# Performance work log

Measured on AMD Instinct MI355X. Metric: run time of the kernel, lower is better.

## Reference

```python
import jax, jax.numpy as jnp
import numpy as np

B, L, D, K = 8, 1024, 1024, 128
VOCAB, N_ATOM_FEAT, N_TIMESTEPS = 160, 512, 1000
NEG = jnp.finfo(jnp.float32).min
SCALING = K ** (-0.5)


def setup_inputs() -> dict:
    key = jax.random.key(0)
    ks = jax.random.split(key, 14)
    inp = {}
    # forward args
    inp["token_id"] = jax.random.randint(ks[0], (B, L), 0, VOCAB)  # 0 => padding
    inp["node_attr"] = jax.random.randint(ks[1], (B, L, 9), 0, N_ATOM_FEAT)
    inp["is_molecule"] = jax.random.randint(ks[2], (B,), 0, 2).astype(bool)
    inp["pos"] = jax.random.normal(ks[3], (B, L, 3), jnp.float32) * 10.0
    inp["time_step"] = jax.random.randint(ks[4], (B, L), 0, N_TIMESTEPS)
    # learned parameters
    inp["embed_table"] = jax.random.normal(ks[5], (VOCAB, D), jnp.float32) * 0.02
    inp["atom_feat_table"] = jax.random.normal(ks[6], (N_ATOM_FEAT, D), jnp.float32) * 0.02
    inp["time_table"] = jax.random.normal(ks[7], (N_TIMESTEPS, D), jnp.float32) * 0.02
    inp["time_w1"] = jax.random.normal(ks[8], (D, D), jnp.float32) * (D ** -0.5)
    inp["time_b1"] = jnp.zeros((D,), jnp.float32)
    inp["time_w2"] = jax.random.normal(ks[9], (D, D), jnp.float32) * (D ** -0.5)
    inp["time_b2"] = jnp.zeros((D,), jnp.float32)
    inp["pos_emb_w"] = jax.random.normal(ks[10], (1, K), jnp.float32)          # Linear(1 -> K), no bias
    inp["pos_feature_w"] = jax.random.normal(ks[11], (K, D), jnp.float32) * (K ** -0.5)  # Linear(K -> D), no bias
    return inp


def _pos_emb(pos, padding_mask, pos_emb_w, pos_feature_w):
    # pos: [B,L,3], padding_mask: [B,L] bool
    delta = pos[:, :, None, :] - pos[:, None, :, :]          # [B,L,L,3]
    dist = 1.0 / (jnp.linalg.norm(delta, axis=-1) + 1.0)     # [B,L,L]
    # masked_fill on key side (expand_mask) and query side (padding_mask)
    mask = padding_mask[:, None, :] | padding_mask[:, :, None]
    dist = jnp.where(mask, NEG, dist)
    # value projection: Linear(1->K) on per-atom radial norm, zeroed at padding
    pe = jnp.linalg.norm(pos, axis=-1, keepdims=True) @ pos_emb_w  # [B,L,K]
    pe = jnp.where(padding_mask[:, :, None], 0.0, pe)
    attn = jax.nn.softmax(dist * SCALING, axis=-1)            # [B,L,L]
    pfe = jnp.einsum("bqk,bkc->bqc", attn, pe)                 # [B,L,K]
    pfe = pfe @ pos_feature_w                                  # [B,L,D]
    return jnp.where(padding_mask[:, :, None], 0.0, pfe)


def reference(token_id, node_attr, is_molecule, pos, time_step,
              embed_table, atom_feat_table, time_table,
              time_w1, time_b1, time_w2, time_b2,
              pos_emb_w, pos_feature_w):
    padding_mask = token_id == 0                               # [B,L]
    x = embed_table[token_id]                                  # [B,L,D]
    # 2D atom features: embed cols 1: and sum over feature axis
    atom_emb = atom_feat_table[node_attr[:, :, 1:]].sum(axis=-2)  # [B,L,D]
    atom_emb = jnp.where(is_molecule[:, None, None], atom_emb, 0.0)
    x = x + atom_emb
    # time step encoder: learnable embedding + Linear-SiLU-Linear MLP
    t = time_table[time_step]                                   # [B,L,D]
    time_embed = jax.nn.silu(t @ time_w1 + time_b1) @ time_w2 + time_b2
    x = x + time_embed
    # pairwise 3D positional embedding (softmax attention over 1/(r+1))
    x = x + _pos_emb(pos, padding_mask, pos_emb_w, pos_feature_w)
    return x, padding_mask
```

## Files before the change

### kernel.cpp

```cpp
#include <hip/hip_runtime.h>
#include <hip/hip_bf16.h>
#include <math.h>

#define BB 8
#define LL 1024
#define DD 1024
#define KK 128
#define NTS 1000
#define SCALE 0.08838834764831845f

typedef __attribute__((ext_vector_type(8))) short short8;
typedef __attribute__((ext_vector_type(4))) float f32x4;

__device__ __forceinline__ unsigned short f2bf(float x) {
    __hip_bfloat16 h = __float2bfloat16(x);
    return *reinterpret_cast<unsigned short*>(&h);
}
__device__ __forceinline__ float bf2f(unsigned short u) {
    return __uint_as_float(((unsigned int)u) << 16);
}

__device__ __forceinline__ void gload_lds16(const void* g, void* l) {
    __builtin_amdgcn_global_load_lds(
        (const __attribute__((address_space(1))) unsigned int*)g,
        (__attribute__((address_space(3))) unsigned int*)l, 16, 0, 0);
}

union SMem {
    float4 keys[LL];
    float  tile[32][33];
};

__device__ __forceinline__ void transpose_tile(
    const float* __restrict__ in, unsigned short* __restrict__ out,
    int idx, SMem& sm)
{
    const int tid = threadIdx.x;
    const int bx = (idx & 31) * 32, by = (idx >> 5) * 32;
    const int tx = tid & 31, ty = tid >> 5;
    #pragma unroll
    for (int r = 0; r < 32; r += 8)
        sm.tile[ty + r][tx] = in[(size_t)(by + ty + r) * DD + bx + tx];
    __syncthreads();
    #pragma unroll
    for (int r = 0; r < 32; r += 8)
        out[(size_t)(bx + ty + r) * DD + by + tx] = f2bf(sm.tile[tx][ty + r]);
    __syncthreads();
}

template<bool AF32>
__device__ __forceinline__ void gemm64(
    const float* __restrict__ Af, const unsigned short* __restrict__ Ab,
    const unsigned short* __restrict__ Bt, const float* __restrict__ bias,
    unsigned short* __restrict__ Cout, int mBase, int nBase, bool do_silu)
{
    __shared__ __align__(16) unsigned short As[2][64 * 64];
    __shared__ __align__(16) unsigned short Bs[2][64 * 64];

    const int tid  = threadIdx.x;
    const int lane = tid & 63, wave = tid >> 6;
    const int wm = wave >> 1, wn = wave & 1;
    const int quad = lane >> 4, l16 = lane & 15;
    const int c0 = wave * 2;

    int rowA[2], kEl[2], rAc[2];
    #pragma unroll
    for (int i = 0; i < 2; ++i) {
        const int c   = c0 + i;
        const int o   = c * 1024 + lane * 16;
        const int row = o >> 7;
        const int lin = o ^ ((row & 7) << 4);
        rowA[i] = row;
        kEl[i]  = (lin & 127) >> 1;
        if (AF32) {
            int r = mBase + row;
            rAc[i] = r < NTS ? r : NTS - 1;
        }
    }

    f32x4 acc[2][2];
    #pragma unroll
    for (int i = 0; i < 2; ++i)
        #pragma unroll
        for (int j = 0; j < 2; ++j)
            acc[i][j] = (f32x4){0.f, 0.f, 0.f, 0.f};

    float4 pa[2][2];

    if (AF32) {
        #pragma unroll
        for (int i = 0; i < 2; ++i) {
            const float* p = Af + (size_t)rAc[i] * DD + kEl[i];
            pa[i][0] = *(const float4*)p;
            pa[i][1] = *(const float4*)(p + 4);
        }
    } else {
        #pragma unroll
        for (int i = 0; i < 2; ++i)
            gload_lds16(Ab + (size_t)(mBase + rowA[i]) * DD + kEl[i],
                        (char*)&As[0][0] + (c0 + i) * 1024);
    }
    #pragma unroll
    for (int i = 0; i < 2; ++i)
        gload_lds16(Bt + (size_t)(nBase + rowA[i]) * DD + kEl[i],
                    (char*)&Bs[0][0] + (c0 + i) * 1024);
    asm volatile("s_waitcnt vmcnt(0)" ::: "memory");
    if (AF32) {
        #pragma unroll
        for (int i = 0; i < 2; ++i) {
            short8 s;
            s[0] = f2bf(pa[i][0].x); s[1] = f2bf(pa[i][0].y);
            s[2] = f2bf(pa[i][0].z); s[3] = f2bf(pa[i][0].w);
            s[4] = f2bf(pa[i][1].x); s[5] = f2bf(pa[i][1].y);
            s[6] = f2bf(pa[i][1].z); s[7] = f2bf(pa[i][1].w);
            *(short8*)((char*)&As[0][0] + (c0 + i) * 1024 + lane * 16) = s;
        }
    }
    __syncthreads();

    int buf = 0;
    for (int t = 0; t < 16; ++t) {
        const int kn = (t + 1) * 64;
        if (t < 15) {
            if (AF32) {
                #pragma unroll
                for (int i = 0; i < 2; ++i) {
                    const float* p = Af + (size_t)rAc[i] * DD + kn + kEl[i];
                    pa[i][0] = *(const float4*)p;
                    pa[i][1] = *(const float4*)(p + 4);
                }
            } else {
                #pragma unroll
                for (int i = 0; i < 2; ++i)
                    gload_lds16(Ab + (size_t)(mBase + rowA[i]) * DD + kn + kEl[i],
                                (char*)&As[buf ^ 1][0] + (c0 + i) * 1024);
            }
            #pragma unroll
            for (int i = 0; i < 2; ++i)
                gload_lds16(Bt + (size_t)(nBase + rowA[i]) * DD + kn + kEl[i],
                            (char*)&Bs[buf ^ 1][0] + (c0 + i) * 1024);
        }

        #pragma unroll
        for (int kk = 0; kk < 64; kk += 32) {
            short8 a[2], b[2];
            #pragma unroll
            for (int i = 0; i < 2; ++i) {
                const int row  = wm * 32 + i * 16 + l16;
                const int byte = ((row << 7) + ((kk + quad * 8) << 1))
                                 ^ ((row & 7) << 4);
                a[i] = *(const short8*)((const char*)&As[buf][0] + byte);
            }
            #pragma unroll
            for (int j = 0; j < 2; ++j) {
                const int row  = wn * 32 + j * 16 + l16;
                const int byte = ((row << 7) + ((kk + quad * 8) << 1))
                                 ^ ((row & 7) << 4);
                b[j] = *(const short8*)((const char*)&Bs[buf][0] + byte);
            }
            #pragma unroll
            for (int i = 0; i < 2; ++i)
                #pragma unroll
                for (int j = 0; j < 2; ++j)
                    acc[i][j] = __builtin_amdgcn_mfma_f32_16x16x32_bf16(
                                    a[i], b[j], acc[i][j], 0, 0, 0);
        }

        if (t < 15) {
            asm volatile("s_waitcnt vmcnt(0)" ::: "memory");
            if (AF32) {
                #pragma unroll
                for (int i = 0; i < 2; ++i) {
                    short8 s;
                    s[0] = f2bf(pa[i][0].x); s[1] = f2bf(pa[i][0].y);
                    s[2] = f2bf(pa[i][0].z); s[3] = f2bf(pa[i][0].w);
                    s[4] = f2bf(pa[i][1].x); s[5] = f2bf(pa[i][1].y);
                    s[6] = f2bf(pa[i][1].z); s[7] = f2bf(pa[i][1].w);
                    *(short8*)((char*)&As[buf ^ 1][0] + (c0 + i) * 1024 + lane * 16) = s;
                }
            }
            __syncthreads();
        }
        buf ^= 1;
    }

    #pragma unroll
    for (int j = 0; j < 2; ++j) {
        const int col = nBase + wn * 32 + j * 16 + l16;
        const float bv = bias[col];
        #pragma unroll
        for (int i = 0; i < 2; ++i) {
            #pragma unroll
            for (int r = 0; r < 4; ++r) {
                const int row = mBase + wm * 32 + i * 16 + quad * 4 + r;
                float val = acc[i][j][r] + bv;
                if (do_silu) val = val / (1.0f + __expf(-val));
                Cout[(size_t)row * DD + col] = f2bf(val);
            }
        }
    }
}

__global__ __launch_bounds__(256) void prep(
    const float* __restrict__ w1,
    const float* __restrict__ w2,
    const float* __restrict__ embed_f,
    const float* __restrict__ atom_f,
    const float* __restrict__ pos_emb_w,
    const float* __restrict__ pos_feature_w,
    const void*  __restrict__ is_mol_raw,
    const int*   __restrict__ token_id,
    const float* __restrict__ pos,
    unsigned short* __restrict__ W1t,
    unsigned short* __restrict__ W2t,
    unsigned short* __restrict__ embed_bf,
    unsigned short* __restrict__ atom_bf,
    float* __restrict__ v,
    int*   __restrict__ is_mol_out,
    float* __restrict__ sSg)
{
    __shared__ SMem sm;
    const int blk = blockIdx.x;
    const int tid = threadIdx.x;

    if (blk < 1024) {
        transpose_tile(w1, W1t, blk, sm);
    } else if (blk < 2048) {
        transpose_tile(w2, W2t, blk - 1024, sm);
    } else if (blk < 2208) {
        const int e = ((blk - 2048) * 256 + tid) * 4;
        float4 vv = *(const float4*)&embed_f[e];
        ushort4 o = { f2bf(vv.x), f2bf(vv.y), f2bf(vv.z), f2bf(vv.w) };
        *(ushort4*)&embed_bf[e] = o;
    } else if (blk < 2720) {
        const int e = ((blk - 2208) * 256 + tid) * 4;
        float4 vv = *(const float4*)&atom_f[e];
        ushort4 o = { f2bf(vv.x), f2bf(vv.y), f2bf(vv.z), f2bf(vv.w) };
        *(ushort4*)&atom_bf[e] = o;
    } else if (blk < 2724) {
        const int d = (blk - 2720) * 256 + tid;
        float acc = 0.0f;
        #pragma unroll 4
        for (int c = 0; c < KK; ++c)
            acc += pos_emb_w[c] * pos_feature_w[c * DD + d];
        v[d] = acc;
    } else if (blk == 2724) {
        if (tid == 0) {
            const int* ip = (const int*)is_mol_raw;
            const unsigned char* cp = (const unsigned char*)is_mol_raw;
            bool all_bin = true;
            for (int i = 0; i < BB; ++i) {
                int x = ip[i];
                if (x != 0 && x != 1) all_bin = false;
            }
            for (int i = 0; i < BB; ++i)
                is_mol_out[i] = all_bin ? (ip[i] != 0) : (cp[i] != 0);
        }
    } else {
        const int ab = blk - 2725;
        const int batch = ab >> 6;
        const int q0 = (ab & 63) * 16;
        const int lane = tid & 63, wave = tid >> 6;

        #pragma unroll
        for (int i = 0; i < 4; ++i) {
            const int k = tid + i * 256;
            const int t = batch * LL + k;
            const float x = pos[t * 3 + 0];
            const float y = pos[t * 3 + 1];
            const float z = pos[t * 3 + 2];
            const int tok = token_id[t];
            const float n = sqrtf(x * x + y * y + z * z);
            sm.keys[k] = make_float4(x, y, z, tok == 0 ? -1.0f : n);
        }
        __syncthreads();

        #pragma unroll
        for (int qi = 0; qi < 4; ++qi) {
            const int ql = wave * 4 + qi;
            const float4 qk = sm.keys[q0 + ql];
            float lsum = 0.0f, lws = 0.0f;
            #pragma unroll 4
            for (int i = 0; i < 16; ++i) {
                const float4 kd = sm.keys[lane + i * 64];
                const float dx = qk.x - kd.x, dy = qk.y - kd.y, dz = qk.z - kd.z;
                const float dn = sqrtf(dx * dx + dy * dy + dz * dz);
                const float e = __expf(SCALE / (dn + 1.0f));
                const bool valid = kd.w >= 0.0f;
                const float ev = valid ? e : 0.0f;
                lsum += ev;
                lws  += ev * (valid ? kd.w : 0.0f);
            }
            #pragma unroll
            for (int off = 32; off > 0; off >>= 1) {
                lsum += __shfl_xor(lsum, off);
                lws  += __shfl_xor(lws,  off);
            }
            if (lane == 0)
                sSg[batch * LL + q0 + ql] = (qk.w < 0.0f) ? 0.0f : (lws / lsum);
        }
    }
}

__global__ __launch_bounds__(256) void gemm1k(
    const float* __restrict__ time_table,
    const unsigned short* __restrict__ W1t,
    const float* __restrict__ b1,
    unsigned short* __restrict__ H)
{
    const int b = (blockIdx.x & 7) * 32 + (blockIdx.x >> 3);
    gemm64<true>(time_table, nullptr, W1t, b1, H,
                 (b >> 4) * 64, (b & 15) * 64, true);
}

__global__ __launch_bounds__(256) void gemm2k(
    const unsigned short* __restrict__ H,
    const unsigned short* __restrict__ W2t,
    const float* __restrict__ b2,
    unsigned short* __restrict__ Ebf)
{
    const int b = (blockIdx.x & 7) * 32 + (blockIdx.x >> 3);
    gemm64<false>(nullptr, H, W2t, b2, Ebf,
                  (b >> 4) * 64, (b & 15) * 64, false);
}

__global__ __launch_bounds__(256) void assemble(
    const int*   __restrict__ token_id,
    const int*   __restrict__ node_attr,
    const int*   __restrict__ time_step,
    const unsigned short* __restrict__ embed_bf,
    const unsigned short* __restrict__ atom_bf,
    const unsigned short* __restrict__ Ebf,
    const float* __restrict__ v,
    const float* __restrict__ sSg,
    const int*   __restrict__ is_mol,
    float* __restrict__ out)
{
    const int blk   = blockIdx.x;
    const int batch = blk >> 7;
    const int q0    = (blk & 127) << 3;
    const int tid   = threadIdx.x;

    const int im   = is_mol[batch];
    const int half = tid >> 7;
    const int tl   = tid & 127;
    const int j    = tl * 8;
    const float4 v0 = *(const float4*)&v[j];
    const float4 v1 = *(const float4*)&v[j + 4];

    #pragma unroll
    for (int qp = 0; qp < 4; ++qp) {
        const int ql  = qp * 2 + half;
        const int t   = batch * LL + q0 + ql;
        const int tok = token_id[t];
        const int ts  = time_step[t];
        const float s = sSg[t];

        float o[8];
        short8 eb = *(const short8*)&embed_bf[(size_t)tok * DD + j];
        #pragma unroll
        for (int d = 0; d < 8; ++d) o[d] = bf2f((unsigned short)eb[d]);

        if (im) {
            #pragma unroll
            for (int f = 1; f < 9; ++f) {
                const int a = node_attr[t * 9 + f];
                short8 ab = *(const short8*)&atom_bf[(size_t)a * DD + j];
                #pragma unroll
                for (int d = 0; d < 8; ++d) o[d] += bf2f((unsigned short)ab[d]);
            }
        }
        short8 er = *(const short8*)&Ebf[(size_t)ts * DD + j];
        #pragma unroll
        for (int d = 0; d < 8; ++d) o[d] += bf2f((unsigned short)er[d]);

        o[0] += s * v0.x; o[1] += s * v0.y; o[2] += s * v0.z; o[3] += s * v0.w;
        o[4] += s * v1.x; o[5] += s * v1.y; o[6] += s * v1.z; o[7] += s * v1.w;

        float4 wlo = {o[0], o[1], o[2], o[3]};
        float4 whi = {o[4], o[5], o[6], o[7]};
        *(float4*)&out[(size_t)t * DD + j]     = wlo;
        *(float4*)&out[(size_t)t * DD + j + 4] = whi;
    }

    if (tid < 8) {
        const int t = batch * LL + q0 + tid;
        out[(size_t)BB * LL * DD + t] = (token_id[t] == 0) ? 1.0f : 0.0f;
    }
}

extern "C" void kernel_launch(void* const* d_in, const int* in_sizes, int n_in,
                              void* d_out, int out_size, void* d_ws, size_t ws_size,
                              hipStream_t stream)
{
    const int*   token_id      = (const int*)  d_in[0];
    const int*   node_attr     = (const int*)  d_in[1];
    const void*  is_mol_raw    = (const void*) d_in[2];
    const float* pos           = (const float*)d_in[3];
    const int*   time_step     = (const int*)  d_in[4];
    const float* embed_table   = (const float*)d_in[5];
    const float* atom_feat     = (const float*)d_in[6];
    const float* time_table    = (const float*)d_in[7];
    const float* w1            = (const float*)d_in[8];
    const float* b1            = (const float*)d_in[9];
    const float* w2            = (const float*)d_in[10];
    const float* b2            = (const float*)d_in[11];
    const float* pos_emb_w     = (const float*)d_in[12];
    const float* pos_feature_w = (const float*)d_in[13];

    float* out = (float*)d_out;
    char*  ws  = (char*)d_ws;

    unsigned short* W1t      = (unsigned short*)(ws);
    unsigned short* Ebf      = (unsigned short*)(ws);
    unsigned short* H        = (unsigned short*)(ws + (2u << 20));
    unsigned short* W2t      = (unsigned short*)(ws + (4u << 20));
    unsigned short* embed_bf = (unsigned short*)(ws + (6u << 20));
    unsigned short* atom_bf  = (unsigned short*)(ws + (6u << 20) + (512u << 10));
    char*           base7    = ws + (7u << 20) + (512u << 10);
    float*          V        = (float*)(base7);
    float*          sSg      = (float*)(base7 + (4u << 10));
    int*            is_mol_r = (int*)  (base7 + (36u << 10));

    prep<<<3237, 256, 0, stream>>>(w1, w2, embed_table, atom_feat,
                                   pos_emb_w, pos_feature_w,
                                   is_mol_raw, token_id, pos,
                                   W1t, W2t, embed_bf, atom_bf,
                                   V, is_mol_r, sSg);

    gemm1k<<<256, 256, 0, stream>>>(time_table, W1t, b1, H);

    gemm2k<<<256, 256, 0, stream>>>(H, W2t, b2, Ebf);

    assemble<<<1024, 256, 0, stream>>>(token_id, node_attr, time_step,
                                       embed_bf, atom_bf, Ebf, V, sSg,
                                       is_mol_r, out);
}
```

Before: 154.2 us.

## Fuse first time-MLP GEMM into prep kernel reading untransposed fp32 W1

Removes the separate W1 transpose and the gemm1 launch. The first GEMM now runs as 256 blocks inside the prep kernel, loading fp32 W1 directly into LDS and converting to bf16 when forming MFMA B fragments. This cuts one launch and the W1 transpose round trip through memory, and lets GEMM1 overlap with the other prep work. In exchange, the B tile is fp32 in LDS (twice the footprint), the per-element strided LDS reads and conversions in the inner loop may add bank conflicts and ALU work, and the larger shared-memory union can lower occupancy for all prep blocks.

```diff
diff --git a/kernel.cpp b/kernel.cpp
--- a/kernel.cpp
+++ b/kernel.cpp
@@ -26,57 +26,58 @@
         (__attribute__((address_space(3))) unsigned int*)l, 16, 0, 0);
 }
 
-union SMem {
+union SMemD1 {
+    struct {
+        unsigned short As[2][64 * 64];
+        float          Bs[2][64 * 64];
+    } g;
     float4 keys[LL];
     float  tile[32][33];
 };
 
 __device__ __forceinline__ void transpose_tile(
     const float* __restrict__ in, unsigned short* __restrict__ out,
-    int idx, SMem& sm)
+    int idx, float (*tile)[33])
 {
     const int tid = threadIdx.x;
     const int bx = (idx & 31) * 32, by = (idx >> 5) * 32;
     const int tx = tid & 31, ty = tid >> 5;
     #pragma unroll
     for (int r = 0; r < 32; r += 8)
-        sm.tile[ty + r][tx] = in[(size_t)(by + ty + r) * DD + bx + tx];
+        tile[ty + r][tx] = in[(size_t)(by + ty + r) * DD + bx + tx];
     __syncthreads();
     #pragma unroll
     for (int r = 0; r < 32; r += 8)
-        out[(size_t)(bx + ty + r) * DD + by + tx] = f2bf(sm.tile[tx][ty + r]);
+        out[(size_t)(bx + ty + r) * DD + by + tx] = f2bf(tile[tx][ty + r]);
     __syncthreads();
 }
 
-template<bool AF32>
-__device__ __forceinline__ void gemm64(
-    const float* __restrict__ Af, const unsigned short* __restrict__ Ab,
-    const unsigned short* __restrict__ Bt, const float* __restrict__ bias,
-    unsigned short* __restrict__ Cout, int mBase, int nBase, bool do_silu)
+__device__ __forceinline__ void gemm1_tile(
+    const float* __restrict__ Af, const float* __restrict__ W1,
+    const float* __restrict__ bias, unsigned short* __restrict__ Cout,
+    int mBase, int nBase, SMemD1& sm)
 {
-    __shared__ __align__(16) unsigned short As[2][64 * 64];
-    __shared__ __align__(16) unsigned short Bs[2][64 * 64];
-
     const int tid  = threadIdx.x;
     const int lane = tid & 63, wave = tid >> 6;
     const int wm = wave >> 1, wn = wave & 1;
     const int quad = lane >> 4, l16 = lane & 15;
-    const int c0 = wave * 2;
-
-    int rowA[2], kEl[2], rAc[2];
+
+    const int cA0 = wave * 2;
+    int rAc[2], kElA[2];
     #pragma unroll
     for (int i = 0; i < 2; ++i) {
-        const int c   = c0 + i;
+        const int c   = cA0 + i;
         const int o   = c * 1024 + lane * 16;
         const int row = o >> 7;
         const int lin = o ^ ((row & 7) << 4);
-        rowA[i] = row;
-        kEl[i]  = (lin & 127) >> 1;
-        if (AF32) {
-            int r = mBase + row;
-            rAc[i] = r < NTS ? r : NTS - 1;
-        }
-    }
+        int r = mBase + row;
+        rAc[i]  = r < NTS ? r : NTS - 1;
+        kElA[i] = (lin & 127) >> 1;
+    }
+
+    const int cB0 = wave * 4;
+    const int rB  = lane >> 4;
+    const int cBb = (lane & 15) * 4;
 
     f32x4 acc[2][2];
     #pragma unroll
@@ -87,34 +88,27 @@
 
     float4 pa[2][2];
 
-    if (AF32) {
-        #pragma unroll
-        for (int i = 0; i < 2; ++i) {
-            const float* p = Af + (size_t)rAc[i] * DD + kEl[i];
-            pa[i][0] = *(const float4*)p;
-            pa[i][1] = *(const float4*)(p + 4);
-        }
-    } else {
-        #pragma unroll
-        for (int i = 0; i < 2; ++i)
-            gload_lds16(Ab + (size_t)(mBase + rowA[i]) * DD + kEl[i],
-                        (char*)&As[0][0] + (c0 + i) * 1024);
-    }
-    #pragma unroll
-    for (int i = 0; i < 2; ++i)
-        gload_lds16(Bt + (size_t)(nBase + rowA[i]) * DD + kEl[i],
-                    (char*)&Bs[0][0] + (c0 + i) * 1024);
+    #pragma unroll
+    for (int i = 0; i < 2; ++i) {
+        const float* p = Af + (size_t)rAc[i] * DD + kElA[i];
+        pa[i][0] = *(const float4*)p;
+        pa[i][1] = *(const float4*)(p + 4);
+    }
+    #pragma unroll
+    for (int i = 0; i < 4; ++i) {
+        const int c = cB0 + i;
+        gload_lds16(W1 + (size_t)(4 * c + rB) * DD + nBase + cBb,
+                    (char*)&sm.g.Bs[0][0] + c * 1024);
+    }
     asm volatile("s_waitcnt vmcnt(0)" ::: "memory");
-    if (AF32) {
-        #pragma unroll
-        for (int i = 0; i < 2; ++i) {
-            short8 s;
-            s[0] = f2bf(pa[i][0].x); s[1] = f2bf(pa[i][0].y);
-            s[2] = f2bf(pa[i][0].z); s[3] = f2bf(pa[i][0].w);
-            s[4] = f2bf(pa[i][1].x); s[5] = f2bf(pa[i][1].y);
-            s[6] = f2bf(pa[i][1].z); s[7] = f2bf(pa[i][1].w);
-            *(short8*)((char*)&As[0][0] + (c0 + i) * 1024 + lane * 16) = s;
-        }
+    #pragma unroll
+    for (int i = 0; i < 2; ++i) {
+        short8 s;
+        s[0] = f2bf(pa[i][0].x); s[1] = f2bf(pa[i][0].y);
+        s[2] = f2bf(pa[i][0].z); s[3] = f2bf(pa[i][0].w);
+        s[4] = f2bf(pa[i][1].x); s[5] = f2bf(pa[i][1].y);
+        s[6] = f2bf(pa[i][1].z); s[7] = f2bf(pa[i][1].w);
+        *(short8*)((char*)&sm.g.As[0][0] + (cA0 + i) * 1024 + lane * 16) = s;
     }
     __syncthreads();
 
@@ -122,23 +116,18 @@
     for (int t = 0; t < 16; ++t) {
         const int kn = (t + 1) * 64;
         if (t < 15) {
-            if (AF32) {
-                #pragma unroll
-                for (int i = 0; i < 2; ++i) {
-                    const float* p = Af + (size_t)rAc[i] * DD + kn + kEl[i];
-                    pa[i][0] = *(const float4*)p;
-                    pa[i][1] = *(const float4*)(p + 4);
-                }
-            } else {
-                #pragma unroll
-                for (int i = 0; i < 2; ++i)
-                    gload_lds16(Ab + (size_t)(mBase + rowA[i]) * DD + kn + kEl[i],
-                                (char*)&As[buf ^ 1][0] + (c0 + i) * 1024);
-            }
-            #pragma unroll
-            for (int i = 0; i < 2; ++i)
-                gload_lds16(Bt + (size_t)(nBase + rowA[i]) * DD + kn + kEl[i],
-                            (char*)&Bs[buf ^ 1][0] + (c0 + i) * 1024);
+            #pragma unroll
+            for (int i = 0; i < 2; ++i) {
+                const float* p = Af + (size_t)rAc[i] * DD + kn + kElA[i];
+                pa[i][0] = *(const float4*)p;
+                pa[i][1] = *(const float4*)(p + 4);
+            }
+            #pragma unroll
+            for (int i = 0; i < 4; ++i) {
+                const int c = cB0 + i;
+                gload_lds16(W1 + (size_t)(kn + 4 * c + rB) * DD + nBase + cBb,
+                            (char*)&sm.g.Bs[buf ^ 1][0] + c * 1024);
+            }
         }
 
         #pragma unroll
@@ -149,14 +138,16 @@
                 const int row  = wm * 32 + i * 16 + l16;
                 const int byte = ((row << 7) + ((kk + quad * 8) << 1))
                                  ^ ((row & 7) << 4);
-                a[i] = *(const short8*)((const char*)&As[buf][0] + byte);
+                a[i] = *(const short8*)((const char*)&sm.g.As[buf][0] + byte);
             }
             #pragma unroll
             for (int j = 0; j < 2; ++j) {
-                const int row  = wn * 32 + j * 16 + l16;
-                const int byte = ((row << 7) + ((kk + quad * 8) << 1))
-                                 ^ ((row & 7) << 4);
-                b[j] = *(const short8*)((const char*)&Bs[buf][0] + byte);
+                const int ncol = wn * 32 + j * 16 + l16;
+                const float* bp = &sm.g.Bs[buf][(kk + quad * 8) * 64 + ncol];
+                short8 bf;
+                #pragma unroll
+                for (int e = 0; e < 8; ++e) bf[e] = f2bf(bp[e * 64]);
+                b[j] = bf;
             }
             #pragma unroll
             for (int i = 0; i < 2; ++i)
@@ -168,16 +159,14 @@
 
         if (t < 15) {
             asm volatile("s_waitcnt vmcnt(0)" ::: "memory");
-            if (AF32) {
-                #pragma unroll
-                for (int i = 0; i < 2; ++i) {
-                    short8 s;
-                    s[0] = f2bf(pa[i][0].x); s[1] = f2bf(pa[i][0].y);
-                    s[2] = f2bf(pa[i][0].z); s[3] = f2bf(pa[i][0].w);
-                    s[4] = f2bf(pa[i][1].x); s[5] = f2bf(pa[i][1].y);
-                    s[6] = f2bf(pa[i][1].z); s[7] = f2bf(pa[i][1].w);
-                    *(short8*)((char*)&As[buf ^ 1][0] + (c0 + i) * 1024 + lane * 16) = s;
-                }
+            #pragma unroll
+            for (int i = 0; i < 2; ++i) {
+                short8 s;
+                s[0] = f2bf(pa[i][0].x); s[1] = f2bf(pa[i][0].y);
+                s[2] = f2bf(pa[i][0].z); s[3] = f2bf(pa[i][0].w);
+                s[4] = f2bf(pa[i][1].x); s[5] = f2bf(pa[i][1].y);
+                s[6] = f2bf(pa[i][1].z); s[7] = f2bf(pa[i][1].w);
+                *(short8*)((char*)&sm.g.As[buf ^ 1][0] + (cA0 + i) * 1024 + lane * 16) = s;
             }
             __syncthreads();
         }
@@ -194,15 +183,17 @@
             for (int r = 0; r < 4; ++r) {
                 const int row = mBase + wm * 32 + i * 16 + quad * 4 + r;
                 float val = acc[i][j][r] + bv;
-                if (do_silu) val = val / (1.0f + __expf(-val));
+                val = val / (1.0f + __expf(-val));
                 Cout[(size_t)row * DD + col] = f2bf(val);
             }
         }
     }
 }
 
-__global__ __launch_bounds__(256) void prep(
+__global__ __launch_bounds__(256) void d1(
+    const float* __restrict__ time_table,
     const float* __restrict__ w1,
+    const float* __restrict__ b1,
     const float* __restrict__ w2,
     const float* __restrict__ embed_f,
     const float* __restrict__ atom_f,
@@ -211,7 +202,7 @@
     const void*  __restrict__ is_mol_raw,
     const int*   __restrict__ token_id,
     const float* __restrict__ pos,
-    unsigned short* __restrict__ W1t,
+    unsigned short* __restrict__ H,
     unsigned short* __restrict__ W2t,
     unsigned short* __restrict__ embed_bf,
     unsigned short* __restrict__ atom_bf,
@@ -219,32 +210,33 @@
     int*   __restrict__ is_mol_out,
     float* __restrict__ sSg)
 {
-    __shared__ SMem sm;
+    __shared__ SMemD1 sm;
     const int blk = blockIdx.x;
     const int tid = threadIdx.x;
 
-    if (blk < 1024) {
-        transpose_tile(w1, W1t, blk, sm);
-    } else if (blk < 2048) {
-        transpose_tile(w2, W2t, blk - 1024, sm);
-    } else if (blk < 2208) {
-        const int e = ((blk - 2048) * 256 + tid) * 4;
+    if (blk < 256) {
+        const int b = (blk & 7) * 32 + (blk >> 3);
+        gemm1_tile(time_table, w1, b1, H, (b >> 4) * 64, (b & 15) * 64, sm);
+    } else if (blk < 1280) {
+        transpose_tile(w2, W2t, blk - 256, sm.tile);
+    } else if (blk < 1440) {
+        const int e = ((blk - 1280) * 256 + tid) * 4;
         float4 vv = *(const float4*)&embed_f[e];
         ushort4 o = { f2bf(vv.x), f2bf(vv.y), f2bf(vv.z), f2bf(vv.w) };
         *(ushort4*)&embed_bf[e] = o;
-    } else if (blk < 2720) {
-        const int e = ((blk - 2208) * 256 + tid) * 4;
+    } else if (blk < 1952) {
+        const int e = ((blk - 1440) * 256 + tid) * 4;
         float4 vv = *(const float4*)&atom_f[e];
         ushort4 o = { f2bf(vv.x), f2bf(vv.y), f2bf(vv.z), f2bf(vv.w) };
         *(ushort4*)&atom_bf[e] = o;
-    } else if (blk < 2724) {
-        const int d = (blk - 2720) * 256 + tid;
+    } else if (blk < 1956) {
+        const int d = (blk - 1952) * 256 + tid;
         float acc = 0.0f;
         #pragma unroll 4
         for (int c = 0; c < KK; ++c)
             acc += pos_emb_w[c] * pos_feature_w[c * DD + d];
         v[d] = acc;
-    } else if (blk == 2724) {
+    } else if (blk == 1956) {
         if (tid == 0) {
             const int* ip = (const int*)is_mol_raw;
             const unsigned char* cp = (const unsigned char*)is_mol_raw;
@@ -257,7 +249,7 @@
                 is_mol_out[i] = all_bin ? (ip[i] != 0) : (cp[i] != 0);
         }
     } else {
-        const int ab = blk - 2725;
+        const int ab = blk - 1957;
         const int batch = ab >> 6;
         const int q0 = (ab & 63) * 16;
         const int lane = tid & 63, wave = tid >> 6;
@@ -302,26 +294,110 @@
     }
 }
 
-__global__ __launch_bounds__(256) void gemm1k(
-    const float* __restrict__ time_table,
-    const unsigned short* __restrict__ W1t,
-    const float* __restrict__ b1,
-    unsigned short* __restrict__ H)
+__global__ __launch_bounds__(256) void gemm2k(
+    const unsigned short* __restrict__ Ab,
+    const unsigned short* __restrict__ Bt,
+    const float* __restrict__ bias,
+    unsigned short* __restrict__ Cout)
 {
+    __shared__ __align__(16) unsigned short As[2][64 * 64];
+    __shared__ __align__(16) unsigned short Bs[2][64 * 64];
+
     const int b = (blockIdx.x & 7) * 32 + (blockIdx.x >> 3);
-    gemm64<true>(time_table, nullptr, W1t, b1, H,
-                 (b >> 4) * 64, (b & 15) * 64, true);
-}
-
-__global__ __launch_bounds__(256) void gemm2k(
-    const unsigned short* __restrict__ H,
-    const unsigned short* __restrict__ W2t,
-    const float* __restrict__ b2,
-    unsigned short* __restrict__ Ebf)
-{
-    const int b = (blockIdx.x & 7) * 32 + (blockIdx.x >> 3);
-    gemm64<false>(nullptr, H, W2t, b2, Ebf,
-                  (b >> 4) * 64, (b & 15) * 64, false);
+    const int mBase = (b >> 4) * 64, nBase = (b & 15) * 64;
+
+    const int tid  = threadIdx.x;
+    const int lane = tid & 63, wave = tid >> 6;
+    const int wm = wave >> 1, wn = wave & 1;
+    const int quad = lane >> 4, l16 = lane & 15;
+    const int c0 = wave * 2;
+
+    int rowA[2], kEl[2];
+    #pragma unroll
+    for (int i = 0; i < 2; ++i) {
+        const int c   = c0 + i;
+        const int o   = c * 1024 + lane * 16;
+        const int row = o >> 7;
+        const int lin = o ^ ((row & 7) << 4);
+        rowA[i] = row;
+        kEl[i]  = (lin & 127) >> 1;
+    }
+
+    f32x4 acc[2][2];
+    #pragma unroll
+    for (int i = 0; i < 2; ++i)
+        #pragma unroll
+        for (int j = 0; j < 2; ++j)
+            acc[i][j] = (f32x4){0.f, 0.f, 0.f, 0.f};
+
+    #pragma unroll
+    for (int i = 0; i < 2; ++i) {
+        gload_lds16(Ab + (size_t)(mBase + rowA[i]) * DD + kEl[i],
+                    (char*)&As[0][0] + (c0 + i) * 1024);
+        gload_lds16(Bt + (size_t)(nBase + rowA[i]) * DD + kEl[i],
+                    (char*)&Bs[0][0] + (c0 + i) * 1024);
+    }
+    asm volatile("s_waitcnt vmcnt(0)" ::: "memory");
+    __syncthreads();
+
+    int buf = 0;
+    for (int t = 0; t < 16; ++t) {
+        const int kn = (t + 1) * 64;
+        if (t < 15) {
+            #pragma unroll
+            for (int i = 0; i < 2; ++i) {
+                gload_lds16(Ab + (size_t)(mBase + rowA[i]) * DD + kn + kEl[i],
+                            (char*)&As[buf ^ 1][0] + (c0 + i) * 1024);
+                gload_lds16(Bt + (size_t)(nBase + rowA[i]) * DD + kn + kEl[i],
+                            (char*)&Bs[buf ^ 1][0] + (c0 + i) * 1024);
+            }
+        }
+
+        #pragma unroll
+        for (int kk = 0; kk < 64; kk += 32) {
+            short8 a[2], bb[2];
+            #pragma unroll
+            for (int i = 0; i < 2; ++i) {
+                const int row  = wm * 32 + i * 16 + l16;
+                const int byte = ((row << 7) + ((kk + quad * 8) << 1))
+                                 ^ ((row & 7) << 4);
+                a[i] = *(const short8*)((const char*)&As[buf][0] + byte);
+            }
+            #pragma unroll
+            for (int j = 0; j < 2; ++j) {
+                const int row  = wn * 32 + j * 16 + l16;
+                const int byte = ((row << 7) + ((kk + quad * 8) << 1))
+                                 ^ ((row & 7) << 4);
+                bb[j] = *(const short8*)((const char*)&Bs[buf][0] + byte);
+            }
+            #pragma unroll
+            for (int i = 0; i < 2; ++i)
+                #pragma unroll
+                for (int j = 0; j < 2; ++j)
+                    acc[i][j] = __builtin_amdgcn_mfma_f32_16x16x32_bf16(
+                                    a[i], bb[j], acc[i][j], 0, 0, 0);
+        }
+
+        if (t < 15) {
+            asm volatile("s_waitcnt vmcnt(0)" ::: "memory");
+            __syncthreads();
+        }
+        buf ^= 1;
+    }
+
+    #pragma unroll
+    for (int j = 0; j < 2; ++j) {
+        const int col = nBase + wn * 32 + j * 16 + l16;
+        const float bv = bias[col];
+        #pragma unroll
+        for (int i = 0; i < 2; ++i) {
+            #pragma unroll
+            for (int r = 0; r < 4; ++r) {
+                const int row = mBase + wm * 32 + i * 16 + quad * 4 + r;
+                Cout[(size_t)row * DD + col] = f2bf(acc[i][j][r] + bv);
+            }
+        }
+    }
 }
 
 __global__ __launch_bounds__(256) void assemble(
@@ -411,7 +487,6 @@
     float* out = (float*)d_out;
     char*  ws  = (char*)d_ws;
 
-    unsigned short* W1t      = (unsigned short*)(ws);
     unsigned short* Ebf      = (unsigned short*)(ws);
     unsigned short* H        = (unsigned short*)(ws + (2u << 20));
     unsigned short* W2t      = (unsigned short*)(ws + (4u << 20));
@@ -422,13 +497,10 @@
     float*          sSg      = (float*)(base7 + (4u << 10));
     int*            is_mol_r = (int*)  (base7 + (36u << 10));
 
-    prep<<<3237, 256, 0, stream>>>(w1, w2, embed_table, atom_feat,
-                                   pos_emb_w, pos_feature_w,
-                                   is_mol_raw, token_id, pos,
-                                   W1t, W2t, embed_bf, atom_bf,
-                                   V, is_mol_r, sSg);
-
-    gemm1k<<<256, 256, 0, stream>>>(time_table, W1t, b1, H);
+    d1<<<2469, 256, 0, stream>>>(time_table, w1, b1, w2, embed_table,
+                                 atom_feat, pos_emb_w, pos_feature_w,
+                                 is_mol_raw, token_id, pos,
+                                 H, W2t, embed_bf, atom_bf, V, is_mol_r, sSg);
 
     gemm2k<<<256, 256, 0, stream>>>(H, W2t, b2, Ebf);
 
```

Measured after the change: 146.5 us. 1.05x faster.
